# Performance work log

Hardware: AMD Instinct MI355X
Metric: run time of the kernel (lower is better)

Reference implementation:

```python
import jax, jax.numpy as jnp
import numpy as np

SIZE = 512
WIDTH_TILES = 1
N_STROKES = 16
STROKE_WIDTH = 0.04
N_SAMPLES = 32


def setup_inputs() -> dict:
    key = jax.random.key(0)
    # matches torch.rand(n_free,4,2)*0.6+0.2 init
    control_points = jax.random.uniform(key, (N_STROKES, 4, 2), dtype=jnp.float32) * 0.6 + 0.2
    ys = jnp.linspace(0.0, 1.0, SIZE)
    xs = jnp.linspace(0.0, 1.0, SIZE * WIDTH_TILES)
    grid_y, grid_x = jnp.meshgrid(ys, xs, indexing='ij')
    pixel_grid = jnp.stack([grid_x, grid_y], axis=-1).reshape(-1, 2).astype(jnp.float32)  # [HW,2]
    return {"control_points": control_points, "pixel_grid": pixel_grid}


def _bezier3_samples(curves):
    # curves: [S,4,2] -> [S,N_SAMPLES,2]
    ts = jnp.linspace(0.0, 1.0, N_SAMPLES, dtype=curves.dtype)
    t = ts[None, :, None]
    mt = 1.0 - t
    p0, p1, p2, p3 = (curves[:, k:k + 1, :] for k in range(4))
    return mt ** 3 * p0 + 3 * mt ** 2 * t * p1 + 3 * mt * t ** 2 * p2 + t ** 3 * p3


def reference(control_points, pixel_grid):
    pts = jnp.clip(control_points, 0.0, 1.0)  # all_strokes(), symmetric=False, no groups
    pts_flat = _bezier3_samples(pts).reshape(-1, 2)  # [P,2], P = S*N_SAMPLES
    sharpness = float(N_SAMPLES) * 8.0
    # pairwise pixel-to-sample distances: [HW,P]
    diff = pixel_grid[:, None, :] - pts_flat[None, :, :]
    dist = jnp.sqrt(jnp.sum(diff * diff, axis=-1))
    # softmin via logsumexp
    min_dist = -jax.scipy.special.logsumexp(-sharpness * dist, axis=-1) / sharpness  # [HW]
    coverage = jax.nn.sigmoid((STROKE_WIDTH - min_dist) * (8.0 / STROKE_WIDTH))
    return (1.0 - coverage).reshape(SIZE, SIZE * WIDTH_TILES)[None]  # (1,H,W)
```

## Files before the change

### kernel.cpp

```cpp
#include <hip/hip_runtime.h>


#define SIZE    512
#define NPAIRS  256
#define NGRP    64
#define MARGIN  0.05f
#define LOG2E   1.4426950408889634f
#define C2      (256.0f * LOG2E)

typedef float v2f __attribute__((ext_vector_type(2)));
typedef float v4f __attribute__((ext_vector_type(4)));

__device__ __forceinline__ float sqrt_raw(float x) { return __builtin_amdgcn_sqrtf(x); }
__device__ __forceinline__ float exp2_raw(float x) { return __builtin_amdgcn_exp2f(x); }
__device__ __forceinline__ float log2_raw(float x) { return __builtin_amdgcn_logf(x); }
__device__ __forceinline__ float rcp_raw(float x)  { return __builtin_amdgcn_rcpf(x); }
__device__ __forceinline__ float clamp01(float x)  { return fminf(fmaxf(x, 0.0f), 1.0f); }

__global__ __launch_bounds__(256) void bezier_glyph_kernel(
    const float* __restrict__ cp,
    const float* __restrict__ grid,
    float* __restrict__ out)
{
    __shared__ v4f sxy[NPAIRS];
    __shared__ v2f sp2[NPAIRS];
    __shared__ v4f sbox[NGRP];
    __shared__ v2f srep[NGRP];

    const int tid = threadIdx.x;

    {
        float px[2], py[2], pq[2];
#pragma unroll
        for (int k = 0; k < 2; ++k) {
            const int i = 2 * tid + k;
            const int stroke = i >> 5, samp = i & 31;
            const float t  = (float)samp * (1.0f / 31.0f);
            const float mt = 1.0f - t;
            const float b0 = mt * mt * mt;
            const float b1 = 3.0f * mt * mt * t;
            const float b2 = 3.0f * mt * t * t;
            const float b3 = t * t * t;
            const float* p = cp + stroke * 8;
            px[k] = b0 * clamp01(p[0]) + b1 * clamp01(p[2]) + b2 * clamp01(p[4]) + b3 * clamp01(p[6]);
            py[k] = b0 * clamp01(p[1]) + b1 * clamp01(p[3]) + b2 * clamp01(p[5]) + b3 * clamp01(p[7]);
            pq[k] = px[k] * px[k] + py[k] * py[k];
        }
        sxy[tid] = (v4f){px[0], px[1], py[0], py[1]};
        sp2[tid] = (v2f){pq[0], pq[1]};
    }
    __syncthreads();

    if (tid < NGRP) {
        float lox = 1e30f, loy = 1e30f, hix = -1e30f, hiy = -1e30f;
#pragma unroll
        for (int k = 0; k < 4; ++k) {
            const v4f a = sxy[(tid << 2) + k];
            lox = fminf(lox, fminf(a.x, a.y));
            hix = fmaxf(hix, fmaxf(a.x, a.y));
            loy = fminf(loy, fminf(a.z, a.w));
            hiy = fmaxf(hiy, fmaxf(a.z, a.w));
        }
        sbox[tid] = (v4f){lox, loy, hix, hiy};
        const v4f am = sxy[(tid << 2) + 2];
        srep[tid] = (v2f){am.x, am.z};
    }
    __syncthreads();

    const int lane = tid & 63;
    const int wv   = tid >> 6;
    const int x = (blockIdx.x << 4) + (tid & 15);
    const int y = (blockIdx.y << 4) + (tid >> 4);
    const float2 g = reinterpret_cast<const float2*>(grid)[y * SIZE + x];

    const float inv511 = 1.0f / 511.0f;
    const float rx0 = (float)(blockIdx.x << 4) * inv511;
    const float rx1 = (float)((blockIdx.x << 4) + 15) * inv511;
    const float ry0 = (float)((blockIdx.y << 4) + (wv << 2)) * inv511;
    const float ry1 = (float)((blockIdx.y << 4) + (wv << 2) + 3) * inv511;
    const float cxr = 0.5f * (rx0 + rx1);
    const float cyr = 0.5f * (ry0 + ry1);
    const float hdx = 0.5f * (rx1 - rx0), hdy = 0.5f * (ry1 - ry0);
    const float hd  = sqrt_raw(hdx * hdx + hdy * hdy);

    float dc, db2;
    {
        const v2f r = srep[lane];
        const float dcx = cxr - r.x, dcy = cyr - r.y;
        dc = sqrt_raw(dcx * dcx + dcy * dcy);
        const v4f b = sbox[lane];
        const float bdx = fmaxf(fmaxf(b.x - rx1, rx0 - b.z), 0.0f);
        const float bdy = fmaxf(fmaxf(b.y - ry1, ry0 - b.w), 0.0f);
        db2 = bdx * bdx + bdy * bdy;
    }
    float mdc = dc;
#pragma unroll
    for (int s = 1; s < 64; s <<= 1) mdc = fminf(mdc, __shfl_xor(mdc, s));
    const float ub  = mdc + hd;
    const float tau = ub + MARGIN;
    const unsigned long long mask = __ballot(db2 < tau * tau);

    const float n2gx = -2.0f * g.x;
    const float n2gy = -2.0f * g.y;
    const float g2   = g.x * g.x + g.y * g.y;
    const v2f   g2v  = {g2, g2};
    const float bias = C2 * ub;

    float s0 = 0.0f, s1 = 0.0f;
    {
        unsigned long long mm = mask;
        while (mm) {
            const int gi = __ffsll(mm) - 1;
            mm &= mm - 1;
            const int base = gi << 2;
#pragma unroll
            for (int k = 0; k < 4; ++k) {
                const v4f a = sxy[base + k];
                const v2f q = sp2[base + k];
                const v2f u = (v2f){a.x, a.y} * n2gx + ((v2f){a.z, a.w} * n2gy + q);
                const v2f d2v = u + g2v;
                const float da = sqrt_raw(fmaxf(d2v.x, 0.0f));
                const float db = sqrt_raw(fmaxf(d2v.y, 0.0f));
                s0 += exp2_raw(__builtin_fmaf(-C2, da, bias));
                s1 += exp2_raw(__builtin_fmaf(-C2, db, bias));
            }
        }
    }
    const float s = s0 + s1;

    const float min_dist = ub - log2_raw(s) * (1.0f / C2);
    const float z  = (0.04f - min_dist) * 200.0f;
    const float ez = exp2_raw(z * LOG2E);
    out[y * SIZE + x] = rcp_raw(1.0f + ez);
}

extern "C" void kernel_launch(void* const* d_in, const int* in_sizes, int n_in,
                              void* d_out, int out_size, void* d_ws, size_t ws_size,
                              hipStream_t stream) {
    const float* cp   = (const float*)d_in[0];
    const float* grid = (const float*)d_in[1];
    float* out = (float*)d_out;

    dim3 grid_dim(SIZE / 16, SIZE / 16);
    bezier_glyph_kernel<<<grid_dim, 256, 0, stream>>>(cp, grid, out);
}
```

Measured before the change: 65.36 us.

## Add exact per-pixel min-distance prepass to tighten culling and logsumexp bias

Adds a cheap first pass over candidate groups that computes each pixel's exact minimum squared distance using only FMAs. The wave-wide maximum of that distance becomes a tighter culling radius for the expensive sqrt/exp2 loop, and the per-pixel minimum replaces the coarse upper bound as the logsumexp bias. Each group now also has two representative points, which tightens the initial bound. The trade-off is an extra LDS scan over the first-pass groups and extra shuffles, in exchange for skipping more groups in the transcendental loop.

Result: no change. 66.06 us (+1.1%).

```diff
diff --git a/kernel.cpp b/kernel.cpp
--- a/kernel.cpp
+++ b/kernel.cpp
@@ -25,7 +25,7 @@
     __shared__ v4f sxy[NPAIRS];
     __shared__ v2f sp2[NPAIRS];
     __shared__ v4f sbox[NGRP];
-    __shared__ v2f srep[NGRP];
+    __shared__ v4f srep[NGRP];
 
     const int tid = threadIdx.x;
 
@@ -62,8 +62,9 @@
             hiy = fmaxf(hiy, fmaxf(a.z, a.w));
         }
         sbox[tid] = (v4f){lox, loy, hix, hiy};
-        const v4f am = sxy[(tid << 2) + 2];
-        srep[tid] = (v2f){am.x, am.z};
+        const v4f a1 = sxy[(tid << 2) + 1];
+        const v4f a3 = sxy[(tid << 2) + 3];
+        srep[tid] = (v4f){a1.x, a1.z, a3.x, a3.z};
     }
     __syncthreads();
 
@@ -85,9 +86,12 @@
 
     float dc, db2;
     {
-        const v2f r = srep[lane];
-        const float dcx = cxr - r.x, dcy = cyr - r.y;
-        dc = sqrt_raw(dcx * dcx + dcy * dcy);
+        const v4f r = srep[lane];
+        const float d1x = cxr - r.x, d1y = cyr - r.y;
+        const float d2x = cxr - r.z, d2y = cyr - r.w;
+        const float dd1 = d1x * d1x + d1y * d1y;
+        const float dd2 = d2x * d2x + d2y * d2y;
+        dc = sqrt_raw(fminf(dd1, dd2));
         const v4f b = sbox[lane];
         const float bdx = fmaxf(fmaxf(b.x - rx1, rx0 - b.z), 0.0f);
         const float bdy = fmaxf(fmaxf(b.y - ry1, ry0 - b.w), 0.0f);
@@ -96,19 +100,45 @@
     float mdc = dc;
 #pragma unroll
     for (int s = 1; s < 64; s <<= 1) mdc = fminf(mdc, __shfl_xor(mdc, s));
-    const float ub  = mdc + hd;
-    const float tau = ub + MARGIN;
-    const unsigned long long mask = __ballot(db2 < tau * tau);
+    const float ub   = mdc + hd;
+    const float tau1 = ub + MARGIN;
+    const unsigned long long mask1 = __ballot(db2 < tau1 * tau1);
 
     const float n2gx = -2.0f * g.x;
     const float n2gy = -2.0f * g.y;
     const float g2   = g.x * g.x + g.y * g.y;
     const v2f   g2v  = {g2, g2};
-    const float bias = C2 * ub;
+
+    float m0 = 1e30f, m1 = 1e30f;
+    {
+        unsigned long long mm = mask1;
+        while (mm) {
+            const int gi = __ffsll(mm) - 1;
+            mm &= mm - 1;
+            const int base = gi << 2;
+#pragma unroll
+            for (int k = 0; k < 4; ++k) {
+                const v4f a = sxy[base + k];
+                const v2f q = sp2[base + k];
+                const v2f u = (v2f){a.x, a.y} * n2gx + ((v2f){a.z, a.w} * n2gy + q);
+                m0 = fminf(m0, u.x);
+                m1 = fminf(m1, u.y);
+            }
+        }
+    }
+    const float d2min = fmaxf(fminf(m0, m1) + g2, 0.0f);
+    const float dmin  = sqrt_raw(d2min);
+    const float bias  = C2 * dmin;
+
+    float dmax = dmin;
+#pragma unroll
+    for (int s = 1; s < 64; s <<= 1) dmax = fmaxf(dmax, __shfl_xor(dmax, s));
+    const float tau2 = dmax + MARGIN;
+    const unsigned long long mask2 = __ballot(db2 < tau2 * tau2);
 
     float s0 = 0.0f, s1 = 0.0f;
     {
-        unsigned long long mm = mask;
+        unsigned long long mm = mask2;
         while (mm) {
             const int gi = __ffsll(mm) - 1;
             mm &= mm - 1;
@@ -128,7 +158,7 @@
     }
     const float s = s0 + s1;
 
-    const float min_dist = ub - log2_raw(s) * (1.0f / C2);
+    const float min_dist = dmin - log2_raw(s) * (1.0f / C2);
     const float z  = (0.04f - min_dist) * 200.0f;
     const float ez = exp2_raw(z * LOG2E);
     out[y * SIZE + x] = rcp_raw(1.0f + ez);
```

## Use 8x8 wave tiles, two-point group reps, and skip far tiles early

Applied to the files above, without the earlier changes.

Each wave now covers an 8x8 pixel tile instead of a 16x4 strip. This tightens its bounding region and fixes the half-diagonal to a constant. Each group's representative point is now the nearer of two samples, which gives a tighter upper bound on the distance. A wave-wide minimum of the box distances lets tiles farther than about 0.095 from every group write 1.0 and exit before any exp/sqrt work. The early exit rests on the output saturating to 1 far from the strokes, which holds only approximately: coverage there is tiny but not exactly zero.

New measurement: 63.62 us. 1.03x faster.

```diff
diff --git a/kernel.cpp b/kernel.cpp
--- a/kernel.cpp
+++ b/kernel.cpp
@@ -7,6 +7,7 @@
 #define MARGIN  0.05f
 #define LOG2E   1.4426950408889634f
 #define C2      (256.0f * LOG2E)
+#define FART2   0.009025f
 
 typedef float v2f __attribute__((ext_vector_type(2)));
 typedef float v4f __attribute__((ext_vector_type(4)));
@@ -25,7 +26,7 @@
     __shared__ v4f sxy[NPAIRS];
     __shared__ v2f sp2[NPAIRS];
     __shared__ v4f sbox[NGRP];
-    __shared__ v2f srep[NGRP];
+    __shared__ v4f srep[NGRP];
 
     const int tid = threadIdx.x;
 
@@ -62,41 +63,47 @@
             hiy = fmaxf(hiy, fmaxf(a.z, a.w));
         }
         sbox[tid] = (v4f){lox, loy, hix, hiy};
-        const v4f am = sxy[(tid << 2) + 2];
-        srep[tid] = (v2f){am.x, am.z};
+        const v4f a1 = sxy[(tid << 2) + 1];
+        const v4f a3 = sxy[(tid << 2) + 3];
+        srep[tid] = (v4f){a1.x, a1.z, a3.x, a3.z};
     }
     __syncthreads();
 
     const int lane = tid & 63;
     const int wv   = tid >> 6;
-    const int x = (blockIdx.x << 4) + (tid & 15);
-    const int y = (blockIdx.y << 4) + (tid >> 4);
+    const int px0 = (blockIdx.x << 4) + ((wv & 1) << 3);
+    const int py0 = (blockIdx.y << 4) + ((wv & 2) << 2);
+    const int x = px0 + (lane & 7);
+    const int y = py0 + (lane >> 3);
     const float2 g = reinterpret_cast<const float2*>(grid)[y * SIZE + x];
 
     const float inv511 = 1.0f / 511.0f;
-    const float rx0 = (float)(blockIdx.x << 4) * inv511;
-    const float rx1 = (float)((blockIdx.x << 4) + 15) * inv511;
-    const float ry0 = (float)((blockIdx.y << 4) + (wv << 2)) * inv511;
-    const float ry1 = (float)((blockIdx.y << 4) + (wv << 2) + 3) * inv511;
+    const float rx0 = (float)px0 * inv511, rx1 = (float)(px0 + 7) * inv511;
+    const float ry0 = (float)py0 * inv511, ry1 = (float)(py0 + 7) * inv511;
     const float cxr = 0.5f * (rx0 + rx1);
     const float cyr = 0.5f * (ry0 + ry1);
-    const float hdx = 0.5f * (rx1 - rx0), hdy = 0.5f * (ry1 - ry0);
-    const float hd  = sqrt_raw(hdx * hdx + hdy * hdy);
+    const float hd  = 0.009686f;
 
-    float dc, db2;
-    {
-        const v2f r = srep[lane];
-        const float dcx = cxr - r.x, dcy = cyr - r.y;
-        dc = sqrt_raw(dcx * dcx + dcy * dcy);
-        const v4f b = sbox[lane];
-        const float bdx = fmaxf(fmaxf(b.x - rx1, rx0 - b.z), 0.0f);
-        const float bdy = fmaxf(fmaxf(b.y - ry1, ry0 - b.w), 0.0f);
-        db2 = bdx * bdx + bdy * bdy;
+    const v4f b = sbox[lane];
+    const float bdx = fmaxf(fmaxf(b.x - rx1, rx0 - b.z), 0.0f);
+    const float bdy = fmaxf(fmaxf(b.y - ry1, ry0 - b.w), 0.0f);
+    const float db2 = bdx * bdx + bdy * bdy;
+
+    float mdb = db2;
+#pragma unroll
+    for (int s = 1; s < 64; s <<= 1) mdb = fminf(mdb, __shfl_xor(mdb, s));
+    if (mdb > FART2) {
+        out[y * SIZE + x] = 1.0f;
+        return;
     }
-    float mdc = dc;
+
+    const v4f r = srep[lane];
+    const float d1x = cxr - r.x, d1y = cyr - r.y;
+    const float d2x = cxr - r.z, d2y = cyr - r.w;
+    float dc = sqrt_raw(fminf(d1x * d1x + d1y * d1y, d2x * d2x + d2y * d2y));
 #pragma unroll
-    for (int s = 1; s < 64; s <<= 1) mdc = fminf(mdc, __shfl_xor(mdc, s));
-    const float ub  = mdc + hd;
+    for (int s = 1; s < 64; s <<= 1) dc = fminf(dc, __shfl_xor(dc, s));
+    const float ub  = dc + hd;
     const float tau = ub + MARGIN;
     const unsigned long long mask = __ballot(db2 < tau * tau);
 
```
